# Kernel tuning notes

Measured on AMD Instinct MI355X. Metric: run time of the kernel, lower is better.

Reference implementation:

```python
import jax, jax.numpy as jnp
import numpy as np

N_GRID = 128
DX = 1.0 / N_GRID
INV_DX = float(N_GRID)
DT = 1e-4
P_VOL = (DX * 0.5) ** 2
P_RHO = 1.0
P_MASS = P_VOL * P_RHO
E_MOD, NU = 1000.0, 0.2
MU_0 = E_MOD / (2.0 * (1.0 + NU))
LAMBDA_0 = E_MOD * NU / ((1.0 + NU) * (1.0 - 2.0 * NU))
N_PART = 1_000_000


def setup_inputs() -> dict:
    key = jax.random.key(0)
    k1, k2, k3, k4, k5 = jax.random.split(key, 5)
    # particles strictly inside the domain so the 3x3 stencil stays in-grid
    x = 0.1 + 0.8 * jax.random.uniform(k1, (N_PART, 2), jnp.float32)
    v = 0.5 * jax.random.normal(k2, (N_PART, 2), jnp.float32)
    C = 0.1 * jax.random.normal(k3, (N_PART, 2, 2), jnp.float32)
    F = jnp.eye(2, dtype=jnp.float32)[None] + 0.01 * jax.random.normal(k4, (N_PART, 2, 2), jnp.float32)
    material = jax.random.randint(k5, (N_PART,), 0, 3, jnp.int32)
    Jp = jnp.ones((N_PART,), jnp.float32)
    return {"x": x, "v": v, "C": C, "F": F, "material": material, "Jp": Jp}


def mpm_step(x, v, C, F, material, Jp):
    # --- particle kinematics / constitutive model ---
    base = jnp.floor(x * INV_DX - 0.5).astype(jnp.int32)          # (N,2)
    fx = x * INV_DX - base.astype(x.dtype)                        # (N,2)
    w = jnp.stack([0.5 * (1.5 - fx) ** 2,
                   0.75 - (fx - 1.0) ** 2,
                   0.5 * (fx - 0.5) ** 2], axis=0)                # (3,N,2)

    F = F + DT * jnp.einsum('nij,njk->nik', C, F)
    m0 = material == 0
    m2 = material == 2
    h = jnp.where(material == 1, 0.3, jnp.exp(10.0 * (1.0 - Jp)))
    mu = jnp.where(m0, 0.0, MU_0 * h)
    lam = LAMBDA_0 * h

    U, sig, Vh = jnp.linalg.svd(F)                                # batched 2x2 SVD
    clamped = jnp.clip(sig, 1.0 - 2.5e-2, 1.0 + 4.5e-3)
    Jp = jnp.where(m2, Jp * jnp.prod(sig / clamped, axis=-1), Jp)
    sig = jnp.where(m2[:, None], clamped, sig)
    J = jnp.prod(sig, axis=-1)

    eye = jnp.eye(2, dtype=F.dtype)
    F_liquid = eye[None] * jnp.sqrt(J)[:, None, None]             # J**(1/n_dim), n_dim=2
    F_snow = jnp.einsum('nij,nj,njk->nik', U, sig, Vh)
    F = jnp.where(m0[:, None, None], F_liquid,
                  jnp.where(m2[:, None, None], F_snow, F))

    R = jnp.einsum('nij,njk->nik', U, Vh)
    stress = (2.0 * mu[:, None, None] * jnp.einsum('nij,nkj->nik', F - R, F)
              + eye[None] * (lam * J * (J - 1.0))[:, None, None])
    stress = (-DT * P_VOL * 4.0 * INV_DX ** 2) * stress
    affine = stress + P_MASS * C                                  # (N,2,2)

    mom = P_MASS * v - jnp.einsum('nij,nj->ni', affine, x)        # (N,2)

    # --- P2G scatter over 3x3 stencil ---
    grid_v = jnp.zeros((N_GRID * N_GRID, 2), x.dtype)
    grid_m = jnp.zeros((N_GRID * N_GRID,), x.dtype)
    grid_aff = jnp.zeros((N_GRID * N_GRID, 2, 2), x.dtype)
    for i in range(3):
        for j in range(3):
            weight = w[i, :, 0] * w[j, :, 1]                      # (N,)
            idx = (base[:, 0] + i) * N_GRID + (base[:, 1] + j)
            grid_v = grid_v.at[idx].add(weight[:, None] * mom)
            grid_aff = grid_aff.at[idx].add(weight[:, None, None] * affine)
            grid_m = grid_m.at[idx].add(weight * P_MASS)
    grid_v = grid_v.reshape(N_GRID, N_GRID, 2)
    grid_m = grid_m.reshape(N_GRID, N_GRID)
    grid_aff = grid_aff.reshape(N_GRID, N_GRID, 2, 2)

    gi = jnp.arange(N_GRID, dtype=x.dtype)
    grid_x = jnp.stack(jnp.meshgrid(gi, gi, indexing='ij'), axis=-1) * DX   # (G,G,2)
    grid_v = grid_v + jnp.einsum('abij,abj->abi', grid_aff, grid_x)

    # --- grid normalization, gravity, boundary clamps ---
    nonempty = grid_m > 0
    safe_m = jnp.where(nonempty, grid_m, 1.0)
    grid_v = jnp.where(nonempty[..., None], grid_v / safe_m[..., None], grid_v)
    grid_v = grid_v.at[:, :, 1].add(jnp.where(nonempty, -DT * 50.0, 0.0))

    row = jnp.arange(N_GRID)
    vx, vy = grid_v[..., 0], grid_v[..., 1]
    vx = jnp.where(row[:, None] < 3, jnp.maximum(vx, 0.0), vx)
    vx = jnp.where(row[:, None] >= N_GRID - 2, jnp.minimum(vx, 0.0), vx)
    vy = jnp.where(row[None, :] < 3, jnp.maximum(vy, 0.0), vy)
    vy = jnp.where(row[None, :] >= N_GRID - 2, jnp.minimum(vy, 0.0), vy)
    grid_v = jnp.stack([vx, vy], axis=-1)

    # --- G2P gather over 3x3 stencil ---
    new_v = jnp.zeros_like(v)
    new_C = jnp.zeros_like(C)
    for i in range(3):
        for j in range(3):
            weight = w[i, :, 0] * w[j, :, 1]
            g_v = grid_v[base[:, 0] + i, base[:, 1] + j]          # (N,2)
            node = (base + jnp.array([i, j], base.dtype)).astype(x.dtype) * DX
            new_v = new_v + weight[:, None] * g_v
            new_C = new_C + weight[:, None, None] * g_v[:, :, None] * node[:, None, :]
    new_C = (new_C - new_v[:, :, None] * x[:, None, :]) * (4.0 * INV_DX ** 2)

    x_new = x + DT * new_v
    return x_new, new_v, new_C, F, material, Jp


def reference(x, v, C, F, material, Jp):
    return mpm_step(x, v, C, F, material, Jp)
```

## Files before the change

### kernel.cpp

```cpp
#include <hip/hip_runtime.h>

#define NPART 1000000
#define NGRID 128
#define NNODES (NGRID * NGRID)
#define NBINS 64
#define BINCAP 26624
#define SUBW 18
#define SUBN (SUBW * SUBW)
#define P2G_SUB 8
#define P2G_THREADS 512
#define PS_CHUNK 4
#define PS_BLOCKS 977

#define FPSCALE 281474976710656.0f
#define FPINV   3.552713678800501e-15
#define WSCALE  16777216.0f
#define WINV    5.9604644775390625e-8

#define OUT_X   0
#define OUT_V   2000000
#define OUT_C   4000000
#define OUT_F   8000000
#define OUT_MAT 12000000
#define OUT_JP  13000000

__device__ __forceinline__ void quad_weights(float fx, float w[3]) {
    w[0] = 0.5f * (1.5f - fx) * (1.5f - fx);
    w[1] = 0.75f - (fx - 1.0f) * (fx - 1.0f);
    w[2] = 0.5f * (fx - 0.5f) * (fx - 0.5f);
}

struct PhysOut {
    float o00, o01, o10, o11;
    float aff00, aff01, aff10, aff11;
    float mom0, mom1;
    float jp_new;
};

__device__ __forceinline__ PhysOut particle_phys(
    float2 xx, float2 vv, float4 Cm, float4 Fin, int mat, float jp)
{
    const float DT = 1e-4f;
    const float P_MASS = 1.52587890625e-05f;
    const float MU_0 = (float)(1000.0 / (2.0 * 1.2));
    const float LAMBDA_0 = (float)(200.0 / 0.72);
    const float SCALE = -1e-4f;

    float F00 = Fin.x + DT * (Cm.x * Fin.x + Cm.y * Fin.z);
    float F01 = Fin.y + DT * (Cm.x * Fin.y + Cm.y * Fin.w);
    float F10 = Fin.z + DT * (Cm.z * Fin.x + Cm.w * Fin.z);
    float F11 = Fin.w + DT * (Cm.z * Fin.y + Cm.w * Fin.w);

    float h = (mat == 1) ? 0.3f : expf(10.0f * (1.0f - jp));
    float mu = (mat == 0) ? 0.0f : MU_0 * h;
    float lam = LAMBDA_0 * h;

    float Es = 0.5f * (F00 + F11), Fs = 0.5f * (F00 - F11);
    float Gs = 0.5f * (F01 + F10), Hs = 0.5f * (F10 - F01);
    float q2 = Es * Es + Hs * Hs;
    float r2 = Fs * Fs + Gs * Gs;
    float Qs = sqrtf(q2);
    float Rs = sqrtf(r2);
    float s1 = Qs + Rs, s2 = Qs - Rs;
    float cdif = 1.0f, sdif = 0.0f;
    if (q2 > 1e-30f) { float rq = 1.0f / Qs; cdif = Es * rq; sdif = Hs * rq; }
    float csum = 1.0f, ssum = 0.0f;
    if (r2 > 1e-30f) { float rr = 1.0f / Rs; csum = Fs * rr; ssum = Gs * rr; }
    float cucv = 0.5f * (cdif + csum);
    float susv = 0.5f * (cdif - csum);
    float cusv = 0.5f * (ssum - sdif);
    float sucv = 0.5f * (ssum + sdif);

    float c1 = fminf(fmaxf(s1, 1.0f - 2.5e-2f), 1.0f + 4.5e-3f);
    float c2 = fminf(fmaxf(s2, 1.0f - 2.5e-2f), 1.0f + 4.5e-3f);
    float jp_new = jp;
    float sg1 = s1, sg2 = s2;
    if (mat == 2) {
        jp_new = jp * (s1 / c1) * (s2 / c2);
        sg1 = c1;
        sg2 = c2;
    }
    float J = sg1 * sg2;

    float R00 = cdif, R01 = -sdif;
    float R10 = sdif, R11 = cdif;

    float o00, o01, o10, o11;
    if (mat == 0) {
        float sq = sqrtf(J);
        o00 = sq; o01 = 0.0f; o10 = 0.0f; o11 = sq;
    } else if (mat == 2) {
        o00 = sg1 * cucv + sg2 * susv;
        o01 = sg1 * cusv - sg2 * sucv;
        o10 = sg1 * sucv - sg2 * cusv;
        o11 = sg1 * susv + sg2 * cucv;
    } else {
        o00 = F00; o01 = F01; o10 = F10; o11 = F11;
    }

    float A00 = o00 - R00, A01 = o01 - R01, A10 = o10 - R10, A11 = o11 - R11;
    float S00 = A00 * o00 + A01 * o01;
    float S01 = A00 * o10 + A01 * o11;
    float S10 = A10 * o00 + A11 * o01;
    float S11 = A10 * o10 + A11 * o11;
    float ljj = lam * J * (J - 1.0f);

    PhysOut po;
    po.o00 = o00; po.o01 = o01; po.o10 = o10; po.o11 = o11;
    po.aff00 = SCALE * (2.0f * mu * S00 + ljj) + P_MASS * Cm.x;
    po.aff01 = SCALE * (2.0f * mu * S01)       + P_MASS * Cm.y;
    po.aff10 = SCALE * (2.0f * mu * S10)       + P_MASS * Cm.z;
    po.aff11 = SCALE * (2.0f * mu * S11 + ljj) + P_MASS * Cm.w;
    po.mom0 = P_MASS * vv.x - (po.aff00 * xx.x + po.aff01 * xx.y);
    po.mom1 = P_MASS * vv.y - (po.aff10 * xx.x + po.aff11 * xx.y);
    po.jp_new = jp_new;
    return po;
}

__device__ __forceinline__ int tile_of(float2 xx) {
    int b0 = (int)floorf(xx.x * 128.0f - 0.5f);
    int b1 = (int)floorf(xx.y * 128.0f - 0.5f);
    return ((b0 >> 4) << 3) | (b1 >> 4);
}

__global__ __launch_bounds__(256) void phys_scatter_kernel(
    const float2* __restrict__ x, const float2* __restrict__ v,
    const float4* __restrict__ C, const float4* __restrict__ F,
    const int* __restrict__ material, const float* __restrict__ Jp,
    int* __restrict__ binCursor, float* __restrict__ out, float4* __restrict__ rec)
{
    __shared__ int lh[NBINS];
    __shared__ int lbase[NBINS];
    int tid = threadIdx.x;
    if (tid < NBINS) lh[tid] = 0;
    __syncthreads();
    int base = blockIdx.x * (256 * PS_CHUNK);

    float2 xs[PS_CHUNK], vs[PS_CHUNK];
    float4 Cs[PS_CHUNK], Fs[PS_CHUNK];
    float jps[PS_CHUNK];
    int ms[PS_CHUNK], pk[PS_CHUNK];

    #pragma unroll
    for (int c = 0; c < PS_CHUNK; ++c) {
        int n = base + c * 256 + tid;
        if (n < NPART) {
            xs[c] = x[n]; vs[c] = v[n]; Cs[c] = C[n]; Fs[c] = F[n];
            ms[c] = material[n]; jps[c] = Jp[n];
            int t = tile_of(xs[c]);
            int r = atomicAdd(&lh[t], 1);
            pk[c] = (t << 16) | r;
        } else pk[c] = -1;
    }
    __syncthreads();
    if (tid < NBINS) {
        int c = lh[tid];
        lbase[tid] = c ? atomicAdd(&binCursor[tid], c) : 0;
    }
    __syncthreads();

    #pragma unroll
    for (int c = 0; c < PS_CHUNK; ++c) {
        if (pk[c] < 0) continue;
        int n = base + c * 256 + tid;
        PhysOut po = particle_phys(xs[c], vs[c], Cs[c], Fs[c], ms[c], jps[c]);
        ((float4*)(out + OUT_F))[n] = make_float4(po.o00, po.o01, po.o10, po.o11);
        out[OUT_MAT + n] = (float)ms[c];
        out[OUT_JP + n] = po.jp_new;
        int t = pk[c] >> 16, r = pk[c] & 0xffff;
        int pos = t * BINCAP + lbase[t] + r;
        rec[2 * pos]     = make_float4(xs[c].x, xs[c].y, po.mom0, po.mom1);
        rec[2 * pos + 1] = make_float4(po.aff00, po.aff01, po.aff10, po.aff11);
    }
}

__global__ __launch_bounds__(P2G_THREADS) void p2g_kernel(
    const float4* __restrict__ rec, const int* __restrict__ binCursor,
    float* __restrict__ part)
{
    __shared__ unsigned long long s_v0[SUBN], s_v1[SUBN];
    __shared__ unsigned int s_m[SUBN];
    int tid = threadIdx.x;
    int tile = blockIdx.x >> 3;
    int sub  = blockIdx.x & (P2G_SUB - 1);
    for (int i = tid; i < SUBN; i += P2G_THREADS) {
        s_v0[i] = 0ull; s_v1[i] = 0ull; s_m[i] = 0u;
    }
    __syncthreads();
    int start = tile * BINCAP;
    int cnt = binCursor[tile];
    int t0 = (tile >> 3) << 4;
    int t1 = (tile & 7) << 4;
    const float DX = 1.0f / 128.0f;

    for (int p = sub * P2G_THREADS + tid; p < cnt; p += P2G_SUB * P2G_THREADS) {
        float4 r0 = rec[2 * (start + p)];
        float4 r1 = rec[2 * (start + p) + 1];
        float xg0 = r0.x * 128.0f, xg1 = r0.y * 128.0f;
        int b0 = (int)floorf(xg0 - 0.5f), b1 = (int)floorf(xg1 - 0.5f);
        float fx0 = xg0 - (float)b0, fx1 = xg1 - (float)b1;
        float wx[3], wy[3];
        quad_weights(fx0, wx);
        quad_weights(fx1, wy);
        int l0 = b0 - t0, l1 = b1 - t1;
        #pragma unroll
        for (int i = 0; i < 3; ++i) {
            float nx0 = (float)(b0 + i) * DX;
            #pragma unroll
            for (int j = 0; j < 3; ++j) {
                float wt = wx[i] * wy[j];
                float nx1 = (float)(b1 + j) * DX;
                int l = (l0 + i) * SUBW + (l1 + j);
                long long q0 = (long long)(wt * (r0.z + r1.x * nx0 + r1.y * nx1) * FPSCALE);
                long long q1 = (long long)(wt * (r0.w + r1.z * nx0 + r1.w * nx1) * FPSCALE);
                unsigned int qm = (unsigned int)(wt * WSCALE);
                atomicAdd(&s_v0[l], (unsigned long long)q0);
                atomicAdd(&s_v1[l], (unsigned long long)q1);
                atomicAdd(&s_m[l], qm);
            }
        }
    }
    __syncthreads();
    float* slab = part + (size_t)blockIdx.x * (3 * SUBN);
    for (int l = tid; l < SUBN; l += P2G_THREADS) {
        slab[l]            = (float)((double)(long long)s_v0[l] * FPINV);
        slab[SUBN + l]     = (float)((double)(long long)s_v1[l] * FPINV);
        slab[2 * SUBN + l] = (float)((double)s_m[l] * WINV);
    }
}

__global__ __launch_bounds__(256) void grid_kernel(
    const float* __restrict__ part, float2* __restrict__ gvn)
{
    int idx = blockIdx.x * blockDim.x + threadIdx.x;
    if (idx >= NNODES) return;
    const float P_MASS = 1.52587890625e-05f;
    int gi = idx >> 7, gj = idx & 127;
    int li = gi & 15, lj = gj & 15, ti = gi >> 4, tj = gj >> 4;

    int tis[2], l0s[2]; int ni = 1; tis[0] = ti; l0s[0] = li;
    if (li < 2 && ti > 0) { tis[1] = ti - 1; l0s[1] = li + 16; ni = 2; }
    int tjs[2], l1s[2]; int nj = 1; tjs[0] = tj; l1s[0] = lj;
    if (lj < 2 && tj > 0) { tjs[1] = tj - 1; l1s[1] = lj + 16; nj = 2; }

    float s0 = 0.f, s1 = 0.f, sw = 0.f;
    for (int a = 0; a < ni; ++a) {
        for (int b = 0; b < nj; ++b) {
            int tile2 = tis[a] * 8 + tjs[b];
            int l = l0s[a] * SUBW + l1s[b];
            const float* sb = part + (size_t)(tile2 * P2G_SUB) * (3 * SUBN) + l;
            #pragma unroll
            for (int sub = 0; sub < P2G_SUB; ++sub) {
                s0 += sb[0];
                s1 += sb[SUBN];
                sw += sb[2 * SUBN];
                sb += 3 * SUBN;
            }
        }
    }
    float m = sw * P_MASS;
    if (m > 0.f) {
        float rm = 1.0f / m;
        s0 *= rm;
        s1 *= rm;
        s1 -= 5e-3f;
    }
    if (gi < 3) s0 = fmaxf(s0, 0.0f);
    if (gi >= NGRID - 2) s0 = fminf(s0, 0.0f);
    if (gj < 3) s1 = fmaxf(s1, 0.0f);
    if (gj >= NGRID - 2) s1 = fminf(s1, 0.0f);
    gvn[idx] = make_float2(s0, s1);
}

__global__ __launch_bounds__(256) void g2p_kernel(
    const float2* __restrict__ x, const float2* __restrict__ gvn,
    float* __restrict__ out)
{
    int n = blockIdx.x * blockDim.x + threadIdx.x;
    if (n >= NPART) return;
    const float DX = 1.0f / 128.0f;
    const float DT = 1e-4f;
    const float K4 = 65536.0f;

    float2 xx = x[n];
    float xg0 = xx.x * 128.0f, xg1 = xx.y * 128.0f;
    int b0 = (int)floorf(xg0 - 0.5f), b1 = (int)floorf(xg1 - 0.5f);
    float fx0 = xg0 - (float)b0, fx1 = xg1 - (float)b1;
    float wx[3], wy[3];
    quad_weights(fx0, wx);
    quad_weights(fx1, wy);

    float nv0 = 0.f, nv1 = 0.f;
    float nC00 = 0.f, nC01 = 0.f, nC10 = 0.f, nC11 = 0.f;
    #pragma unroll
    for (int i = 0; i < 3; ++i) {
        float node0 = (float)(b0 + i) * DX;
        #pragma unroll
        for (int j = 0; j < 3; ++j) {
            float wt = wx[i] * wy[j];
            float2 g = gvn[(b0 + i) * NGRID + (b1 + j)];
            float node1 = (float)(b1 + j) * DX;
            nv0 += wt * g.x;
            nv1 += wt * g.y;
            nC00 += wt * g.x * node0;
            nC01 += wt * g.x * node1;
            nC10 += wt * g.y * node0;
            nC11 += wt * g.y * node1;
        }
    }
    nC00 = (nC00 - nv0 * xx.x) * K4;
    nC01 = (nC01 - nv0 * xx.y) * K4;
    nC10 = (nC10 - nv1 * xx.x) * K4;
    nC11 = (nC11 - nv1 * xx.y) * K4;

    ((float2*)(out + OUT_X))[n] = make_float2(xx.x + DT * nv0, xx.y + DT * nv1);
    ((float2*)(out + OUT_V))[n] = make_float2(nv0, nv1);
    ((float4*)(out + OUT_C))[n] = make_float4(nC00, nC01, nC10, nC11);
}

extern "C" void kernel_launch(void* const* d_in, const int* in_sizes, int n_in,
                              void* d_out, int out_size, void* d_ws, size_t ws_size,
                              hipStream_t stream)
{
    const float2* x = (const float2*)d_in[0];
    const float2* v = (const float2*)d_in[1];
    const float4* C = (const float4*)d_in[2];
    const float4* F = (const float4*)d_in[3];
    const int* material = (const int*)d_in[4];
    const float* Jp = (const float*)d_in[5];
    float* out = (float*)d_out;

    int* binCursor = (int*)d_ws;
    float* part = (float*)((char*)d_ws + 4096);
    float2* gvn = (float2*)((char*)d_ws + (11 << 18));
    float4* rec = (float4*)((char*)d_ws + (4 << 20));

    hipMemsetAsync(binCursor, 0, NBINS * sizeof(int), stream);

    phys_scatter_kernel<<<PS_BLOCKS, 256, 0, stream>>>(x, v, C, F, material, Jp,
                                                       binCursor, out, rec);
    p2g_kernel<<<NBINS * P2G_SUB, P2G_THREADS, 0, stream>>>(rec, binCursor, part);
    grid_kernel<<<NNODES / 256, 256, 0, stream>>>(part, gvn);
    g2p_kernel<<<(NPART + 255) / 256, 256, 0, stream>>>(x, gvn, out);
}
```

Before: 173.4 us.

## Stage binned records in shared memory and parallelize grid reduction across subslabs

The scatter kernel now sorts each block's particle records by tile in shared memory, using a wave prefix scan over bin counts. It then writes them out in contiguous runs per bin, so global stores coalesce instead of scattering. The grid kernel assigns 8 threads per node, one per p2g sub-slab, and combines the partial sums with xor shuffles, raising parallelism from 16K threads. The cost is about 36KB of extra shared memory per scatter block, which may lower occupancy, plus an extra barrier.

```diff
diff --git a/kernel.cpp b/kernel.cpp
--- a/kernel.cpp
+++ b/kernel.cpp
@@ -11,6 +11,7 @@
 #define P2G_THREADS 512
 #define PS_CHUNK 4
 #define PS_BLOCKS 977
+#define PS_PART (256 * PS_CHUNK)
 
 #define FPSCALE 281474976710656.0f
 #define FPINV   3.552713678800501e-15
@@ -130,11 +131,17 @@
     int* __restrict__ binCursor, float* __restrict__ out, float4* __restrict__ rec)
 {
     __shared__ int lh[NBINS];
+    __shared__ int lpre[NBINS];
     __shared__ int lbase[NBINS];
+    __shared__ int s_total;
+    __shared__ float4 srec0[PS_PART];
+    __shared__ float4 srec1[PS_PART];
+    __shared__ int spos[PS_PART];
+
     int tid = threadIdx.x;
     if (tid < NBINS) lh[tid] = 0;
     __syncthreads();
-    int base = blockIdx.x * (256 * PS_CHUNK);
+    int base = blockIdx.x * PS_PART;
 
     float2 xs[PS_CHUNK], vs[PS_CHUNK];
     float4 Cs[PS_CHUNK], Fs[PS_CHUNK];
@@ -155,7 +162,15 @@
     __syncthreads();
     if (tid < NBINS) {
         int c = lh[tid];
-        lbase[tid] = c ? atomicAdd(&binCursor[tid], c) : 0;
+        int inc = c;
+        #pragma unroll
+        for (int d = 1; d < 64; d <<= 1) {
+            int y = __shfl_up(inc, d);
+            if (tid >= d) inc += y;
+        }
+        lpre[tid] = inc - c;
+        if (tid == NBINS - 1) s_total = inc;
+        lbase[tid] = tid * BINCAP + (c ? atomicAdd(&binCursor[tid], c) : 0);
     }
     __syncthreads();
 
@@ -168,9 +183,18 @@
         out[OUT_MAT + n] = (float)ms[c];
         out[OUT_JP + n] = po.jp_new;
         int t = pk[c] >> 16, r = pk[c] & 0xffff;
-        int pos = t * BINCAP + lbase[t] + r;
-        rec[2 * pos]     = make_float4(xs[c].x, xs[c].y, po.mom0, po.mom1);
-        rec[2 * pos + 1] = make_float4(po.aff00, po.aff01, po.aff10, po.aff11);
+        int loc = lpre[t] + r;
+        srec0[loc] = make_float4(xs[c].x, xs[c].y, po.mom0, po.mom1);
+        srec1[loc] = make_float4(po.aff00, po.aff01, po.aff10, po.aff11);
+        spos[loc] = lbase[t] + r;
+    }
+    __syncthreads();
+
+    int total = s_total;
+    for (int k = tid; k < total; k += 256) {
+        int pos = spos[k];
+        rec[2 * pos]     = srec0[k];
+        rec[2 * pos + 1] = srec1[k];
     }
 }
 
@@ -232,7 +256,9 @@
 __global__ __launch_bounds__(256) void grid_kernel(
     const float* __restrict__ part, float2* __restrict__ gvn)
 {
-    int idx = blockIdx.x * blockDim.x + threadIdx.x;
+    int t = blockIdx.x * 256 + threadIdx.x;
+    int idx = t >> 3;
+    int sub = t & 7;
     if (idx >= NNODES) return;
     const float P_MASS = 1.52587890625e-05f;
     int gi = idx >> 7, gj = idx & 127;
@@ -248,28 +274,32 @@
         for (int b = 0; b < nj; ++b) {
             int tile2 = tis[a] * 8 + tjs[b];
             int l = l0s[a] * SUBW + l1s[b];
-            const float* sb = part + (size_t)(tile2 * P2G_SUB) * (3 * SUBN) + l;
-            #pragma unroll
-            for (int sub = 0; sub < P2G_SUB; ++sub) {
-                s0 += sb[0];
-                s1 += sb[SUBN];
-                sw += sb[2 * SUBN];
-                sb += 3 * SUBN;
-            }
-        }
-    }
-    float m = sw * P_MASS;
-    if (m > 0.f) {
-        float rm = 1.0f / m;
-        s0 *= rm;
-        s1 *= rm;
-        s1 -= 5e-3f;
-    }
-    if (gi < 3) s0 = fmaxf(s0, 0.0f);
-    if (gi >= NGRID - 2) s0 = fminf(s0, 0.0f);
-    if (gj < 3) s1 = fmaxf(s1, 0.0f);
-    if (gj >= NGRID - 2) s1 = fminf(s1, 0.0f);
-    gvn[idx] = make_float2(s0, s1);
+            const float* sb = part + (size_t)(tile2 * P2G_SUB + sub) * (3 * SUBN) + l;
+            s0 += sb[0];
+            s1 += sb[SUBN];
+            sw += sb[2 * SUBN];
+        }
+    }
+    #pragma unroll
+    for (int m = 4; m >= 1; m >>= 1) {
+        s0 += __shfl_xor(s0, m);
+        s1 += __shfl_xor(s1, m);
+        sw += __shfl_xor(sw, m);
+    }
+    if (sub == 0) {
+        float m = sw * P_MASS;
+        if (m > 0.f) {
+            float rm = 1.0f / m;
+            s0 *= rm;
+            s1 *= rm;
+            s1 -= 5e-3f;
+        }
+        if (gi < 3) s0 = fmaxf(s0, 0.0f);
+        if (gi >= NGRID - 2) s0 = fminf(s0, 0.0f);
+        if (gj < 3) s1 = fmaxf(s1, 0.0f);
+        if (gj >= NGRID - 2) s1 = fminf(s1, 0.0f);
+        gvn[idx] = make_float2(s0, s1);
+    }
 }
 
 __global__ __launch_bounds__(256) void g2p_kernel(
@@ -340,6 +370,6 @@
     phys_scatter_kernel<<<PS_BLOCKS, 256, 0, stream>>>(x, v, C, F, material, Jp,
                                                        binCursor, out, rec);
     p2g_kernel<<<NBINS * P2G_SUB, P2G_THREADS, 0, stream>>>(rec, binCursor, part);
-    grid_kernel<<<NNODES / 256, 256, 0, stream>>>(part, gvn);
+    grid_kernel<<<(NNODES * 8) / 256, 256, 0, stream>>>(part, gvn);
     g2p_kernel<<<(NPART + 255) / 256, 256, 0, stream>>>(x, gvn, out);
 }
```

After: 173.7 us. No clear change (+0.2%).

## Fuse MPM pipeline into one cooperative persistent kernel with grid syncs

Applied to the files above, without the earlier changes.

Replaces the memset and four separate kernels (phys/scatter, P2G, grid reduce, G2P) with one cooperative kernel of 256x1024 threads that uses grid-wide syncs between phases. P2G sub-tile results are now combined with global 64-bit fixed-point atomics into a raw grid instead of per-sub-block slabs. Each block rebuilds the full 128x128 grid velocity field in LDS (128 KB) so the G2P gather reads from shared memory. This removes launch gaps and the slab reduction, in exchange for four grid barriers, global atomics, redundant per-block grid normalization, and a single block per CU, which limits latency hiding.

```diff
diff --git a/kernel.cpp b/kernel.cpp
--- a/kernel.cpp
+++ b/kernel.cpp
@@ -1,4 +1,7 @@
 #include <hip/hip_runtime.h>
+#include <hip/hip_cooperative_groups.h>
+
+namespace cg = cooperative_groups;
 
 #define NPART 1000000
 #define NGRID 128
@@ -7,10 +10,11 @@
 #define BINCAP 26624
 #define SUBW 18
 #define SUBN (SUBW * SUBW)
-#define P2G_SUB 8
-#define P2G_THREADS 512
-#define PS_CHUNK 4
-#define PS_BLOCKS 977
+#define BLOCKS 256
+#define THREADS 1024
+#define NTHREADS (BLOCKS * THREADS)
+#define CHUNK 4
+#define P2G_SUB 4
 
 #define FPSCALE 281474976710656.0f
 #define FPINV   3.552713678800501e-15
@@ -123,199 +127,198 @@
     return ((b0 >> 4) << 3) | (b1 >> 4);
 }
 
-__global__ __launch_bounds__(256) void phys_scatter_kernel(
+__global__ __launch_bounds__(THREADS, 1) void fused_kernel(
     const float2* __restrict__ x, const float2* __restrict__ v,
     const float4* __restrict__ C, const float4* __restrict__ F,
     const int* __restrict__ material, const float* __restrict__ Jp,
-    int* __restrict__ binCursor, float* __restrict__ out, float4* __restrict__ rec)
+    int* __restrict__ binCursor, float* __restrict__ out,
+    float4* __restrict__ rec, unsigned long long* __restrict__ raw)
 {
-    __shared__ int lh[NBINS];
-    __shared__ int lbase[NBINS];
+    cg::grid_group gg = cg::this_grid();
+
+    __shared__ union {
+        struct { int lh[NBINS]; int lbase[NBINS]; } a;
+        struct { unsigned long long v0[SUBN], v1[SUBN]; unsigned int m[SUBN]; } b;
+        float2 g[NNODES];
+    } sm;
+
     int tid = threadIdx.x;
-    if (tid < NBINS) lh[tid] = 0;
+    int blk = blockIdx.x;
+    int gtid = blk * THREADS + tid;
+
+    unsigned long long* raw_v0 = raw;
+    unsigned long long* raw_v1 = raw + NNODES;
+    unsigned long long* raw_m  = raw + 2 * NNODES;
+
+    for (int i = gtid; i < 3 * NNODES; i += NTHREADS) raw[i] = 0ull;
+    if (gtid < NBINS) binCursor[gtid] = 0;
+    __threadfence();
+    gg.sync();
+
+    if (tid < NBINS) sm.a.lh[tid] = 0;
     __syncthreads();
-    int base = blockIdx.x * (256 * PS_CHUNK);
-
-    float2 xs[PS_CHUNK], vs[PS_CHUNK];
-    float4 Cs[PS_CHUNK], Fs[PS_CHUNK];
-    float jps[PS_CHUNK];
-    int ms[PS_CHUNK], pk[PS_CHUNK];
-
-    #pragma unroll
-    for (int c = 0; c < PS_CHUNK; ++c) {
-        int n = base + c * 256 + tid;
-        if (n < NPART) {
-            xs[c] = x[n]; vs[c] = v[n]; Cs[c] = C[n]; Fs[c] = F[n];
-            ms[c] = material[n]; jps[c] = Jp[n];
-            int t = tile_of(xs[c]);
-            int r = atomicAdd(&lh[t], 1);
-            pk[c] = (t << 16) | r;
-        } else pk[c] = -1;
-    }
-    __syncthreads();
-    if (tid < NBINS) {
-        int c = lh[tid];
-        lbase[tid] = c ? atomicAdd(&binCursor[tid], c) : 0;
-    }
-    __syncthreads();
-
-    #pragma unroll
-    for (int c = 0; c < PS_CHUNK; ++c) {
-        if (pk[c] < 0) continue;
-        int n = base + c * 256 + tid;
-        PhysOut po = particle_phys(xs[c], vs[c], Cs[c], Fs[c], ms[c], jps[c]);
-        ((float4*)(out + OUT_F))[n] = make_float4(po.o00, po.o01, po.o10, po.o11);
-        out[OUT_MAT + n] = (float)ms[c];
-        out[OUT_JP + n] = po.jp_new;
-        int t = pk[c] >> 16, r = pk[c] & 0xffff;
-        int pos = t * BINCAP + lbase[t] + r;
-        rec[2 * pos]     = make_float4(xs[c].x, xs[c].y, po.mom0, po.mom1);
-        rec[2 * pos + 1] = make_float4(po.aff00, po.aff01, po.aff10, po.aff11);
-    }
-}
-
-__global__ __launch_bounds__(P2G_THREADS) void p2g_kernel(
-    const float4* __restrict__ rec, const int* __restrict__ binCursor,
-    float* __restrict__ part)
-{
-    __shared__ unsigned long long s_v0[SUBN], s_v1[SUBN];
-    __shared__ unsigned int s_m[SUBN];
-    int tid = threadIdx.x;
-    int tile = blockIdx.x >> 3;
-    int sub  = blockIdx.x & (P2G_SUB - 1);
-    for (int i = tid; i < SUBN; i += P2G_THREADS) {
-        s_v0[i] = 0ull; s_v1[i] = 0ull; s_m[i] = 0u;
-    }
-    __syncthreads();
-    int start = tile * BINCAP;
-    int cnt = binCursor[tile];
-    int t0 = (tile >> 3) << 4;
-    int t1 = (tile & 7) << 4;
-    const float DX = 1.0f / 128.0f;
-
-    for (int p = sub * P2G_THREADS + tid; p < cnt; p += P2G_SUB * P2G_THREADS) {
-        float4 r0 = rec[2 * (start + p)];
-        float4 r1 = rec[2 * (start + p) + 1];
-        float xg0 = r0.x * 128.0f, xg1 = r0.y * 128.0f;
-        int b0 = (int)floorf(xg0 - 0.5f), b1 = (int)floorf(xg1 - 0.5f);
-        float fx0 = xg0 - (float)b0, fx1 = xg1 - (float)b1;
-        float wx[3], wy[3];
-        quad_weights(fx0, wx);
-        quad_weights(fx1, wy);
-        int l0 = b0 - t0, l1 = b1 - t1;
+
+    {
+        float2 xs[CHUNK], vs[CHUNK];
+        float4 Cs[CHUNK], Fs[CHUNK];
+        float jps[CHUNK];
+        int ms[CHUNK], pk[CHUNK];
+
         #pragma unroll
-        for (int i = 0; i < 3; ++i) {
-            float nx0 = (float)(b0 + i) * DX;
+        for (int c = 0; c < CHUNK; ++c) {
+            int n = gtid + c * NTHREADS;
+            if (n < NPART) {
+                xs[c] = x[n]; vs[c] = v[n]; Cs[c] = C[n]; Fs[c] = F[n];
+                ms[c] = material[n]; jps[c] = Jp[n];
+                int t = tile_of(xs[c]);
+                int r = atomicAdd(&sm.a.lh[t], 1);
+                pk[c] = (t << 16) | r;
+            } else pk[c] = -1;
+        }
+        __syncthreads();
+        if (tid < NBINS) {
+            int c = sm.a.lh[tid];
+            sm.a.lbase[tid] = tid * BINCAP + (c ? atomicAdd(&binCursor[tid], c) : 0);
+        }
+        __syncthreads();
+
+        #pragma unroll
+        for (int c = 0; c < CHUNK; ++c) {
+            if (pk[c] < 0) continue;
+            int n = gtid + c * NTHREADS;
+            PhysOut po = particle_phys(xs[c], vs[c], Cs[c], Fs[c], ms[c], jps[c]);
+            ((float4*)(out + OUT_F))[n] = make_float4(po.o00, po.o01, po.o10, po.o11);
+            out[OUT_MAT + n] = (float)ms[c];
+            out[OUT_JP + n] = po.jp_new;
+            int t = pk[c] >> 16, r = pk[c] & 0xffff;
+            int pos = sm.a.lbase[t] + r;
+            rec[2 * pos]     = make_float4(xs[c].x, xs[c].y, po.mom0, po.mom1);
+            rec[2 * pos + 1] = make_float4(po.aff00, po.aff01, po.aff10, po.aff11);
+        }
+    }
+    __threadfence();
+    gg.sync();
+
+    {
+        int tile = blk >> 2;
+        int sub  = blk & (P2G_SUB - 1);
+        for (int i = tid; i < SUBN; i += THREADS) {
+            sm.b.v0[i] = 0ull; sm.b.v1[i] = 0ull; sm.b.m[i] = 0u;
+        }
+        __syncthreads();
+        int start = tile * BINCAP;
+        int cnt = binCursor[tile];
+        int t0 = (tile >> 3) << 4;
+        int t1 = (tile & 7) << 4;
+        const float DX = 1.0f / 128.0f;
+
+        for (int p = sub * THREADS + tid; p < cnt; p += P2G_SUB * THREADS) {
+            float4 r0 = rec[2 * (start + p)];
+            float4 r1 = rec[2 * (start + p) + 1];
+            float xg0 = r0.x * 128.0f, xg1 = r0.y * 128.0f;
+            int b0 = (int)floorf(xg0 - 0.5f), b1 = (int)floorf(xg1 - 0.5f);
+            float fx0 = xg0 - (float)b0, fx1 = xg1 - (float)b1;
+            float wx[3], wy[3];
+            quad_weights(fx0, wx);
+            quad_weights(fx1, wy);
+            int l0 = b0 - t0, l1 = b1 - t1;
             #pragma unroll
-            for (int j = 0; j < 3; ++j) {
-                float wt = wx[i] * wy[j];
-                float nx1 = (float)(b1 + j) * DX;
-                int l = (l0 + i) * SUBW + (l1 + j);
-                long long q0 = (long long)(wt * (r0.z + r1.x * nx0 + r1.y * nx1) * FPSCALE);
-                long long q1 = (long long)(wt * (r0.w + r1.z * nx0 + r1.w * nx1) * FPSCALE);
-                unsigned int qm = (unsigned int)(wt * WSCALE);
-                atomicAdd(&s_v0[l], (unsigned long long)q0);
-                atomicAdd(&s_v1[l], (unsigned long long)q1);
-                atomicAdd(&s_m[l], qm);
+            for (int i = 0; i < 3; ++i) {
+                float nx0 = (float)(b0 + i) * DX;
+                #pragma unroll
+                for (int j = 0; j < 3; ++j) {
+                    float wt = wx[i] * wy[j];
+                    float nx1 = (float)(b1 + j) * DX;
+                    int l = (l0 + i) * SUBW + (l1 + j);
+                    long long q0 = (long long)(wt * (r0.z + r1.x * nx0 + r1.y * nx1) * FPSCALE);
+                    long long q1 = (long long)(wt * (r0.w + r1.z * nx0 + r1.w * nx1) * FPSCALE);
+                    unsigned int qm = (unsigned int)(wt * WSCALE);
+                    atomicAdd(&sm.b.v0[l], (unsigned long long)q0);
+                    atomicAdd(&sm.b.v1[l], (unsigned long long)q1);
+                    atomicAdd(&sm.b.m[l], qm);
+                }
             }
         }
-    }
-    __syncthreads();
-    float* slab = part + (size_t)blockIdx.x * (3 * SUBN);
-    for (int l = tid; l < SUBN; l += P2G_THREADS) {
-        slab[l]            = (float)((double)(long long)s_v0[l] * FPINV);
-        slab[SUBN + l]     = (float)((double)(long long)s_v1[l] * FPINV);
-        slab[2 * SUBN + l] = (float)((double)s_m[l] * WINV);
-    }
-}
-
-__global__ __launch_bounds__(256) void grid_kernel(
-    const float* __restrict__ part, float2* __restrict__ gvn)
-{
-    int idx = blockIdx.x * blockDim.x + threadIdx.x;
-    if (idx >= NNODES) return;
-    const float P_MASS = 1.52587890625e-05f;
-    int gi = idx >> 7, gj = idx & 127;
-    int li = gi & 15, lj = gj & 15, ti = gi >> 4, tj = gj >> 4;
-
-    int tis[2], l0s[2]; int ni = 1; tis[0] = ti; l0s[0] = li;
-    if (li < 2 && ti > 0) { tis[1] = ti - 1; l0s[1] = li + 16; ni = 2; }
-    int tjs[2], l1s[2]; int nj = 1; tjs[0] = tj; l1s[0] = lj;
-    if (lj < 2 && tj > 0) { tjs[1] = tj - 1; l1s[1] = lj + 16; nj = 2; }
-
-    float s0 = 0.f, s1 = 0.f, sw = 0.f;
-    for (int a = 0; a < ni; ++a) {
-        for (int b = 0; b < nj; ++b) {
-            int tile2 = tis[a] * 8 + tjs[b];
-            int l = l0s[a] * SUBW + l1s[b];
-            const float* sb = part + (size_t)(tile2 * P2G_SUB) * (3 * SUBN) + l;
+        __syncthreads();
+        for (int l = tid; l < SUBN; l += THREADS) {
+            unsigned long long a0 = sm.b.v0[l], a1 = sm.b.v1[l];
+            unsigned long long am = (unsigned long long)sm.b.m[l];
+            if (!(a0 | a1 | am)) continue;
+            int li = l / SUBW, lj = l - li * SUBW;
+            int g0 = t0 + li, g1 = t1 + lj;
+            if (g0 >= NGRID || g1 >= NGRID) continue;
+            int g = g0 * NGRID + g1;
+            atomicAdd(&raw_v0[g], a0);
+            atomicAdd(&raw_v1[g], a1);
+            atomicAdd(&raw_m[g], am);
+        }
+    }
+    __threadfence();
+    gg.sync();
+
+    {
+        const float P_MASS = 1.52587890625e-05f;
+        for (int idx = tid; idx < NNODES; idx += THREADS) {
+            float s0 = (float)((double)(long long)raw_v0[idx] * FPINV);
+            float s1 = (float)((double)(long long)raw_v1[idx] * FPINV);
+            float sw = (float)((double)raw_m[idx] * WINV);
+            int gi = idx >> 7, gj = idx & 127;
+            float m = sw * P_MASS;
+            if (m > 0.f) {
+                float rm = 1.0f / m;
+                s0 *= rm;
+                s1 *= rm;
+                s1 -= 5e-3f;
+            }
+            if (gi < 3) s0 = fmaxf(s0, 0.0f);
+            if (gi >= NGRID - 2) s0 = fminf(s0, 0.0f);
+            if (gj < 3) s1 = fmaxf(s1, 0.0f);
+            if (gj >= NGRID - 2) s1 = fminf(s1, 0.0f);
+            sm.g[idx] = make_float2(s0, s1);
+        }
+        __syncthreads();
+
+        const float DX = 1.0f / 128.0f;
+        const float DT = 1e-4f;
+        const float K4 = 65536.0f;
+
+        for (int n = gtid; n < NPART; n += NTHREADS) {
+            float2 xx = x[n];
+            float xg0 = xx.x * 128.0f, xg1 = xx.y * 128.0f;
+            int b0 = (int)floorf(xg0 - 0.5f), b1 = (int)floorf(xg1 - 0.5f);
+            float fx0 = xg0 - (float)b0, fx1 = xg1 - (float)b1;
+            float wx[3], wy[3];
+            quad_weights(fx0, wx);
+            quad_weights(fx1, wy);
+
+            float nv0 = 0.f, nv1 = 0.f;
+            float nC00 = 0.f, nC01 = 0.f, nC10 = 0.f, nC11 = 0.f;
             #pragma unroll
-            for (int sub = 0; sub < P2G_SUB; ++sub) {
-                s0 += sb[0];
-                s1 += sb[SUBN];
-                sw += sb[2 * SUBN];
-                sb += 3 * SUBN;
+            for (int i = 0; i < 3; ++i) {
+                float node0 = (float)(b0 + i) * DX;
+                #pragma unroll
+                for (int j = 0; j < 3; ++j) {
+                    float wt = wx[i] * wy[j];
+                    float2 g = sm.g[(b0 + i) * NGRID + (b1 + j)];
+                    float node1 = (float)(b1 + j) * DX;
+                    nv0 += wt * g.x;
+                    nv1 += wt * g.y;
+                    nC00 += wt * g.x * node0;
+                    nC01 += wt * g.x * node1;
+                    nC10 += wt * g.y * node0;
+                    nC11 += wt * g.y * node1;
+                }
             }
-        }
-    }
-    float m = sw * P_MASS;
-    if (m > 0.f) {
-        float rm = 1.0f / m;
-        s0 *= rm;
-        s1 *= rm;
-        s1 -= 5e-3f;
-    }
-    if (gi < 3) s0 = fmaxf(s0, 0.0f);
-    if (gi >= NGRID - 2) s0 = fminf(s0, 0.0f);
-    if (gj < 3) s1 = fmaxf(s1, 0.0f);
-    if (gj >= NGRID - 2) s1 = fminf(s1, 0.0f);
-    gvn[idx] = make_float2(s0, s1);
-}
-
-__global__ __launch_bounds__(256) void g2p_kernel(
-    const float2* __restrict__ x, const float2* __restrict__ gvn,
-    float* __restrict__ out)
-{
-    int n = blockIdx.x * blockDim.x + threadIdx.x;
-    if (n >= NPART) return;
-    const float DX = 1.0f / 128.0f;
-    const float DT = 1e-4f;
-    const float K4 = 65536.0f;
-
-    float2 xx = x[n];
-    float xg0 = xx.x * 128.0f, xg1 = xx.y * 128.0f;
-    int b0 = (int)floorf(xg0 - 0.5f), b1 = (int)floorf(xg1 - 0.5f);
-    float fx0 = xg0 - (float)b0, fx1 = xg1 - (float)b1;
-    float wx[3], wy[3];
-    quad_weights(fx0, wx);
-    quad_weights(fx1, wy);
-
-    float nv0 = 0.f, nv1 = 0.f;
-    float nC00 = 0.f, nC01 = 0.f, nC10 = 0.f, nC11 = 0.f;
-    #pragma unroll
-    for (int i = 0; i < 3; ++i) {
-        float node0 = (float)(b0 + i) * DX;
-        #pragma unroll
-        for (int j = 0; j < 3; ++j) {
-            float wt = wx[i] * wy[j];
-            float2 g = gvn[(b0 + i) * NGRID + (b1 + j)];
-            float node1 = (float)(b1 + j) * DX;
-            nv0 += wt * g.x;
-            nv1 += wt * g.y;
-            nC00 += wt * g.x * node0;
-            nC01 += wt * g.x * node1;
-            nC10 += wt * g.y * node0;
-            nC11 += wt * g.y * node1;
-        }
-    }
-    nC00 = (nC00 - nv0 * xx.x) * K4;
-    nC01 = (nC01 - nv0 * xx.y) * K4;
-    nC10 = (nC10 - nv1 * xx.x) * K4;
-    nC11 = (nC11 - nv1 * xx.y) * K4;
-
-    ((float2*)(out + OUT_X))[n] = make_float2(xx.x + DT * nv0, xx.y + DT * nv1);
-    ((float2*)(out + OUT_V))[n] = make_float2(nv0, nv1);
-    ((float4*)(out + OUT_C))[n] = make_float4(nC00, nC01, nC10, nC11);
+            nC00 = (nC00 - nv0 * xx.x) * K4;
+            nC01 = (nC01 - nv0 * xx.y) * K4;
+            nC10 = (nC10 - nv1 * xx.x) * K4;
+            nC11 = (nC11 - nv1 * xx.y) * K4;
+
+            ((float2*)(out + OUT_X))[n] = make_float2(xx.x + DT * nv0, xx.y + DT * nv1);
+            ((float2*)(out + OUT_V))[n] = make_float2(nv0, nv1);
+            ((float4*)(out + OUT_C))[n] = make_float4(nC00, nC01, nC10, nC11);
+        }
+    }
 }
 
 extern "C" void kernel_launch(void* const* d_in, const int* in_sizes, int n_in,
@@ -331,15 +334,13 @@
     float* out = (float*)d_out;
 
     int* binCursor = (int*)d_ws;
-    float* part = (float*)((char*)d_ws + 4096);
-    float2* gvn = (float2*)((char*)d_ws + (11 << 18));
+    unsigned long long* raw = (unsigned long long*)((char*)d_ws + 4096);
     float4* rec = (float4*)((char*)d_ws + (4 << 20));
 
-    hipMemsetAsync(binCursor, 0, NBINS * sizeof(int), stream);
-
-    phys_scatter_kernel<<<PS_BLOCKS, 256, 0, stream>>>(x, v, C, F, material, Jp,
-                                                       binCursor, out, rec);
-    p2g_kernel<<<NBINS * P2G_SUB, P2G_THREADS, 0, stream>>>(rec, binCursor, part);
-    grid_kernel<<<NNODES / 256, 256, 0, stream>>>(part, gvn);
-    g2p_kernel<<<(NPART + 255) / 256, 256, 0, stream>>>(x, gvn, out);
-}
+    void* args[] = {
+        (void*)&x, (void*)&v, (void*)&C, (void*)&F, (void*)&material, (void*)&Jp,
+        (void*)&binCursor, (void*)&out, (void*)&rec, (void*)&raw
+    };
+    hipLaunchCooperativeKernel((const void*)fused_kernel,
+                               dim3(BLOCKS), dim3(THREADS), args, 0, stream);
+}
```

Measured after the change: 563.6 us. 3.25x slower.
